# Optimization experiments

Measured on AMD Instinct MI355X. Metric: run time of the kernel, lower is better.

## Reference

```python
import jax, jax.numpy as jnp
import numpy as np

# ---- quantization constants (8-bit, per-tensor affine; representative values) ----
Q_MAX = 255.0
S_IN, Z_IN = 0.05, 128.0      # block input
S1, Z1 = 0.04, 128.0          # after expand 1x1 + hardswish
S2, Z2 = 0.04, 128.0          # after depthwise 5x5 + hardswish
S_SE1, Z_SE1 = 0.03, 128.0    # SE fc1 output
S_SE2, Z_SE2 = 1.0 / 255.0, 0.0  # SE fc2 hardsigmoid output in [0,1]
S_MUL, Z_MUL = 0.04, 128.0    # SE gated activation
S3, Z3 = 0.05, 128.0          # after project 1x1
S_OUT, Z_OUT = 0.06, 128.0    # after residual add
W_SCALE = 0.01                # symmetric per-tensor weight scale (zero_point = 0)
EXP_C = 576                   # expanded channels (depthwise groups)


def conv(x, w, stride=1, padding=0, groups=1):
    return jax.lax.conv_general_dilated(
        x, w, (stride, stride), [(padding, padding), (padding, padding)],
        feature_group_count=groups, dimension_numbers=('NCHW', 'OIHW', 'NCHW'))


def hardswish(x):
    return x * jnp.clip(x + 3.0, 0.0, 6.0) * (1.0 / 6.0)


def hardsigmoid(x):
    return jnp.clip(x + 3.0, 0.0, 6.0) * (1.0 / 6.0)


def qconv(x_q, w_q, b_q, s_in, z_in, s_out, z_out, stride=1, padding=0, groups=1, act=None):
    """Quantized conv: int-domain accumulation (simulated in fp32), fused activation
    on the dequantized accumulator, then requantize to [0, Q_MAX]."""
    acc = conv(x_q - z_in, w_q, stride, padding, groups) + b_q[None, :, None, None]
    deq = acc * (s_in * W_SCALE)  # dequantize accumulator
    if act == 'hardswish':
        deq = hardswish(deq)
    elif act == 'hardsigmoid':
        deq = hardsigmoid(deq)
    return jnp.clip(deq * (1.0 / s_out) + z_out, 0.0, Q_MAX)


def setup_inputs() -> dict:
    key = jax.random.key(0)
    ks = jax.random.split(key, 11)
    def qw(k, shape):  # int8-style symmetric weights stored as fp32 integers
        return jnp.round(jnp.clip(jax.random.normal(k, shape) * 40.0, -127.0, 127.0))
    def qb(k, n):      # int32-style bias in accumulator domain
        return jnp.round(jax.random.normal(k, (n,)) * 500.0)
    return {
        'x':      jnp.round(jax.random.uniform(ks[0], (64, 96, 28, 28)) * Q_MAX),
        'w_exp':  qw(ks[1], (576, 96, 1, 1)),  'b_exp':  qb(ks[2], 576),
        'w_dw':   qw(ks[3], (576, 1, 5, 5)),   'b_dw':   qb(ks[4], 576),
        'w_se1':  qw(ks[5], (144, 576, 1, 1)), 'b_se1':  qb(ks[6], 144),
        'w_se2':  qw(ks[7], (576, 144, 1, 1)), 'b_se2':  qb(ks[8], 576),
        'w_proj': qw(ks[9], (96, 576, 1, 1)),  'b_proj': qb(ks[10], 96),
    }


def reference(x, w_exp, b_exp, w_dw, b_dw, w_se1, b_se1, w_se2, b_se2, w_proj, b_proj):
    # expand 1x1 (+ hardswish)
    e = qconv(x, w_exp, b_exp, S_IN, Z_IN, S1, Z1, act='hardswish')
    # depthwise 5x5, padding=(5-1)//2=2, groups=expanded (+ hardswish)
    d = qconv(e, w_dw, b_dw, S1, Z1, S2, Z2, padding=2, groups=EXP_C, act='hardswish')
    # squeeze-excitation: global avg pool -> fc1 -> fc2(hardsigmoid) -> quantized mul
    pooled = jnp.mean(d, axis=(2, 3), keepdims=True)  # [N, 576, 1, 1]
    g1 = qconv(pooled, w_se1, b_se1, S2, Z2, S_SE1, Z_SE1)
    g2 = qconv(g1, w_se2, b_se2, S_SE1, Z_SE1, S_SE2, Z_SE2, act='hardsigmoid')
    gated = jnp.clip((g2 - Z_SE2) * (d - Z2) * (S_SE2 * S2 / S_MUL) + Z_MUL, 0.0, Q_MAX)
    # project 1x1 (linear)
    p = qconv(gated, w_proj, b_proj, S_MUL, Z_MUL, S3, Z3)
    # quantized residual add (stride=1, in==out channels -> use_res_connect)
    out = jnp.clip((x - Z_IN) * (S_IN / S_OUT) + (p - Z3) * (S3 / S_OUT) + Z_OUT, 0.0, Q_MAX)
    return out
```

## Files before the change

### kernel.cpp

```cpp
#include <hip/hip_runtime.h>

typedef _Float16 v8h __attribute__((ext_vector_type(8)));
typedef _Float16 v4h __attribute__((ext_vector_type(4)));
typedef _Float16 v2h __attribute__((ext_vector_type(2)));
typedef float v4f __attribute__((ext_vector_type(4)));

#define NB 64
#define CI 96
#define CE 576
#define CO 96
#define HW 784
#define SEC 144

#if defined(__has_builtin)
#if __has_builtin(__builtin_amdgcn_fdot2)
#define HAVE_FDOT2 1
#endif
#endif

__device__ __forceinline__ float fdot2(v2h a, v2h b, float c) {
#ifdef HAVE_FDOT2
  return __builtin_amdgcn_fdot2(a, b, c, false);
#else
  return (float)a[0] * (float)b[0] + ((float)a[1] * (float)b[1] + c);
#endif
}

__device__ __forceinline__ float clampf(float x, float lo, float hi) {
#if defined(__has_builtin)
#if __has_builtin(__builtin_amdgcn_fmed3f)
  return __builtin_amdgcn_fmed3f(x, lo, hi);
#else
  return fminf(fmaxf(x, lo), hi);
#endif
#else
  return fminf(fmaxf(x, lo), hi);
#endif
}

__global__ __launch_bounds__(256) void k0_pack_cvt(const float* __restrict__ x,
                                                   _Float16* __restrict__ x_f,
                                                   const float* __restrict__ w_exp,
                                                   const float* __restrict__ w_proj,
                                                   _Float16* __restrict__ w_exp_h,
                                                   _Float16* __restrict__ w_proj_h) {
  __shared__ _Float16 xl[112][104];
  const int tid = threadIdx.x;

  if (blockIdx.y == NB) {
    for (int i = blockIdx.x * 256 + tid; i < CE * CI; i += 7 * 256) {
      w_exp_h[i]  = (_Float16)w_exp[i];
      w_proj_h[i] = (_Float16)w_proj[i];
    }
    return;
  }

  const int n = blockIdx.y;
  const int hw0 = blockIdx.x * 112;

  for (int idx = tid; idx < CI * 28; idx += 256) {
    int c = idx / 28, seg = idx % 28;
    const float4 v = *(const float4*)&x[(n * CI + c) * HW + hw0 + seg * 4];
    int row = seg * 4;
    xl[row + 0][c] = (_Float16)(v.x - 128.0f);
    xl[row + 1][c] = (_Float16)(v.y - 128.0f);
    xl[row + 2][c] = (_Float16)(v.z - 128.0f);
    xl[row + 3][c] = (_Float16)(v.w - 128.0f);
  }
  __syncthreads();

  for (int idx = tid; idx < 1344; idx += 256) {
    int t_l = idx / 192, rem = idx % 192, s = rem / 64, ln = rem % 64;
    int hw_l = t_l * 16 + (ln & 15), ci = s * 32 + (ln >> 4) * 8;
    v8h o;
#pragma unroll
    for (int j = 0; j < 8; ++j) o[j] = xl[hw_l][ci + j];
    size_t t = (size_t)(blockIdx.x * 7 + t_l);
    *(v8h*)&x_f[(((size_t)n * 49 + t) * 3 + s) * 512 + ln * 8] = o;
  }
}

__global__ __launch_bounds__(512, 8) void k12_fused(const _Float16* __restrict__ x_f,
                                                    const _Float16* __restrict__ w_exp_h,
                                                    const float* __restrict__ b_exp,
                                                    const float* __restrict__ w_dw,
                                                    const float* __restrict__ b_dw,
                                                    _Float16* __restrict__ d_t,
                                                    float* __restrict__ d_sums2) {
  __shared__ _Float16 e_lds[16][18][38];
  __shared__ _Float16 d_tile[16][394];
  __shared__ _Float16 w_pairs[16][5][8];
  const int tid = threadIdx.x;

  const int flat = blockIdx.x + 36 * blockIdx.y + 72 * blockIdx.z;
  const int xcd = flat & 7, slot = flat >> 3;
  const int nl = slot / 72, w72 = slot - nl * 72;
  const int n = xcd * 8 + nl;
  const int h = w72 / 36;
  const int c0 = (w72 - h * 36) * 16;

  {
    unsigned long long* z = (unsigned long long*)&e_lds[0][0][0];
    for (int idx = tid; idx < 16 * 18 * 38 * 2 / 8; idx += 512) z[idx] = 0ull;
  }
  for (int idx = tid; idx < 640; idx += 512) {
    int c = idx / 40, r = idx % 40, dy = r / 8, k = r % 8;
    int tap = (k < 4) ? k : (k - 3);
    w_pairs[c][dy][k] = (_Float16)w_dw[(c0 + c) * 25 + dy * 5 + tap];
  }
  __syncthreads();

  const int wv = tid >> 6, lane = tid & 63;
  const int l15 = lane & 15, q = lane >> 4;

  {
    const _Float16* wrow = &w_exp_h[(c0 + l15) * CI + q * 8];
    v8h a0 = *(const v8h*)(wrow);
    v8h a1 = *(const v8h*)(wrow + 32);
    v8h a2 = *(const v8h*)(wrow + 64);
    float bia3[4], bia2[4];
#pragma unroll
    for (int r = 0; r < 4; ++r) {
      float b = b_exp[c0 + q * 4 + r];
      bia3[r] = fmaf(b, 5.0e-4f, 3.0f);
      bia2[r] = b * (5.0e-4f * 25.0f / 6.0f);
    }

    const int ir0 = 14 * h - 2;
    const _Float16* xb = x_f + (size_t)n * (49 * 3 * 512) + lane * 8;
    int hw0 = (21 * h + wv) * 16 + l15;
    int y = hw0 / 28;
    int xx = hw0 - y * 28;
#pragma unroll
    for (int it = 0; it < 4; ++it) {
      int t_l = wv + it * 8;
      if (t_l < 28) {
        int t = 21 * h + t_l;
        const _Float16* xt = xb + (size_t)t * (3 * 512);
        v8h b0 = *(const v8h*)(xt);
        v8h b1 = *(const v8h*)(xt + 512);
        v8h b2 = *(const v8h*)(xt + 1024);
        v4f acc = (v4f){0.f, 0.f, 0.f, 0.f};
        acc = __builtin_amdgcn_mfma_f32_16x16x32_f16(a0, b0, acc, 0, 0, 0);
        acc = __builtin_amdgcn_mfma_f32_16x16x32_f16(a1, b1, acc, 0, 0, 0);
        acc = __builtin_amdgcn_mfma_f32_16x16x32_f16(a2, b2, acc, 0, 0, 0);
        _Float16* dst = &e_lds[q * 4][y - ir0][6 + xx];
#pragma unroll
        for (int r = 0; r < 4; ++r) {
          float t1  = fmaf(acc[r], 5.0e-4f, bia3[r]);
          float cl  = clampf(t1, 0.0f, 6.0f);
          float a2v = fmaf(acc[r], 5.0e-4f * 25.0f / 6.0f, bia2[r]);
          float ev  = clampf(a2v * cl, -128.0f, 127.0f);
          dst[r * (18 * 38)] = (_Float16)ev;
        }
      }
      xx += 16; y += 4;
      if (xx >= 28) { xx -= 28; ++y; }
    }
  }
  __syncthreads();

  const int c = tid >> 5, l = tid & 31;
  v2h W01[5], W23[5], W12[5], W34[5];
  float W0s[5], W4s[5];
#pragma unroll
  for (int dy = 0; dy < 5; ++dy) {
    W01[dy] = *(const v2h*)&w_pairs[c][dy][0];
    W23[dy] = *(const v2h*)&w_pairs[c][dy][2];
    W12[dy] = *(const v2h*)&w_pairs[c][dy][4];
    W34[dy] = *(const v2h*)&w_pairs[c][dy][6];
    W0s[dy] = (float)W01[dy][0];
    W4s[dy] = (float)W34[dy][1];
  }
  const float bc = b_dw[c0 + c];

#define DW_REQUANT(oo, dvv)                                                   \
  {                                                                           \
    float t1_ = fmaf((oo), 4.0e-4f, 3.0f);                                    \
    float cl_ = clampf(t1_, 0.0f, 6.0f);                                      \
    dvv = clampf((oo) * (4.0e-4f * 25.0f / 6.0f) * cl_, -128.0f, 127.0f);     \
  }

  float csum = 0.0f;
  if (l < 28) {
    const int ry = l >> 1;
    const int bx = (l & 1) * 14;
    v2h P0[5], P1[5], P2[5], P3[5];
#pragma unroll
    for (int dy = 0; dy < 5; ++dy) {
      const _Float16* row = &e_lds[c][ry + dy][bx];
      P0[dy] = *(const v2h*)(row + 4);
      P1[dy] = *(const v2h*)(row + 6);
      P2[dy] = *(const v2h*)(row + 8);
      P3[dy] = *(const v2h*)(row + 10);
    }
#pragma unroll
    for (int xi = 0; xi < 3; ++xi) {
      const int x0 = bx + xi * 4;
      float o0 = bc, o1 = bc, o2 = bc, o3 = bc;
#pragma unroll
      for (int dy = 0; dy < 5; ++dy) {
        o0 = fdot2(P0[dy], W01[dy], o0);
        o0 = fdot2(P1[dy], W23[dy], o0);
        o0 += (float)P2[dy][0] * W4s[dy];
        o1 += (float)P0[dy][1] * W0s[dy];
        o1 = fdot2(P1[dy], W12[dy], o1);
        o1 = fdot2(P2[dy], W34[dy], o1);
        o2 = fdot2(P1[dy], W01[dy], o2);
        o2 = fdot2(P2[dy], W23[dy], o2);
        o2 += (float)P3[dy][0] * W4s[dy];
        o3 += (float)P1[dy][1] * W0s[dy];
        o3 = fdot2(P2[dy], W12[dy], o3);
        o3 = fdot2(P3[dy], W34[dy], o3);
      }
      float d0, d1, d2, d3;
      DW_REQUANT(o0, d0); DW_REQUANT(o1, d1);
      DW_REQUANT(o2, d2); DW_REQUANT(o3, d3);
      csum += (d0 + d1) + (d2 + d3);
      v2h dva, dvb;
      dva[0] = (_Float16)d0; dva[1] = (_Float16)d1;
      dvb[0] = (_Float16)d2; dvb[1] = (_Float16)d3;
      *(v2h*)&d_tile[c][ry * 28 + x0]     = dva;
      *(v2h*)&d_tile[c][ry * 28 + x0 + 2] = dvb;
#pragma unroll
      for (int dy = 0; dy < 5; ++dy) {
        const _Float16* row = &e_lds[c][ry + dy][bx];
        P0[dy] = P2[dy];
        P1[dy] = P3[dy];
        P2[dy] = *(const v2h*)(row + x0 - bx + 12);
        P3[dy] = *(const v2h*)(row + x0 - bx + 14);
      }
    }
    {
      float o0 = bc, o1 = bc;
#pragma unroll
      for (int dy = 0; dy < 5; ++dy) {
        o0 = fdot2(P0[dy], W01[dy], o0);
        o0 = fdot2(P1[dy], W23[dy], o0);
        o0 += (float)P2[dy][0] * W4s[dy];
        o1 += (float)P0[dy][1] * W0s[dy];
        o1 = fdot2(P1[dy], W12[dy], o1);
        o1 = fdot2(P2[dy], W34[dy], o1);
      }
      float d0, d1;
      DW_REQUANT(o0, d0); DW_REQUANT(o1, d1);
      csum += d0 + d1;
      v2h dv; dv[0] = (_Float16)d0; dv[1] = (_Float16)d1;
      *(v2h*)&d_tile[c][ry * 28 + bx + 12] = dv;
    }
  }
#pragma unroll
  for (int m = 16; m >= 1; m >>= 1) csum += __shfl_xor(csum, m);
  if (l == 0) d_sums2[((size_t)h * NB + n) * CE + c0 + c] = csum;

  __syncthreads();
  const size_t obase = ((size_t)n * 72 + (c0 >> 3)) * 784 + 392 * h;
  if (tid < 392) {
    int hw_l = tid;
    v8h o0, o1;
#pragma unroll
    for (int j = 0; j < 8; ++j) { o0[j] = d_tile[j][hw_l]; o1[j] = d_tile[8 + j][hw_l]; }
    *(v8h*)&d_t[(obase + hw_l) * 8] = o0;
    *(v8h*)&d_t[(obase + 784 + hw_l) * 8] = o1;
  }
}

__global__ __launch_bounds__(256) void k3a_fc1(const float* __restrict__ d_sums2,
                                               const float* __restrict__ w_se1,
                                               const float* __restrict__ b_se1,
                                               float* __restrict__ g1) {
  const int tid = threadIdx.x;
  const int wv = tid >> 6, lane = tid & 63;
  const int n = blockIdx.y;
  const int o = blockIdx.x * 4 + wv;
  const float* wrow = &w_se1[o * CE];
  const float* s0 = &d_sums2[(size_t)n * CE];
  const float* s1 = &d_sums2[((size_t)NB + n) * CE];
  float p = 0.f;
#pragma unroll
  for (int s = 0; s < 9; ++s) {
    int cc = lane + s * 64;
    p = fmaf(wrow[cc], s0[cc] + s1[cc], p);
  }
#pragma unroll
  for (int m = 32; m >= 1; m >>= 1) p += __shfl_xor(p, m);
  if (lane == 0) {
    g1[n * SEC + o] = clampf(fmaf(p, 1.0f / 58800.0f,
                                  fmaf(b_se1[o], 1.0f / 75.0f, 128.0f)),
                             0.0f, 255.0f) - 128.0f;
  }
}

__global__ __launch_bounds__(256) void k3b_fc2(const float* __restrict__ g1,
                                               const float* __restrict__ w_se2,
                                               const float* __restrict__ b_se2,
                                               _Float16* __restrict__ g2h) {
  const int tid = threadIdx.x;
  const int wv = tid >> 6, lane = tid & 63;
  const int n = blockIdx.y;
  const int o = blockIdx.x * 4 + wv;
  const float* wrow = &w_se2[o * SEC];
  const float* grow = &g1[n * SEC];
  float p = fmaf(wrow[lane], grow[lane], wrow[lane + 64] * grow[lane + 64]);
  if (lane < 16) p = fmaf(wrow[lane + 128], grow[lane + 128], p);
#pragma unroll
  for (int m = 32; m >= 1; m >>= 1) p += __shfl_xor(p, m);
  if (lane == 0) {
    float t = fmaf(p, 3.0e-4f, fmaf(b_se2[o], 3.0e-4f, 3.0f));
    g2h[n * CE + o] = (_Float16)(clampf(t, 0.0f, 6.0f) * (1.0f / 6.0f));
  }
}

__global__ __launch_bounds__(192) void k4_proj(const _Float16* __restrict__ d_t,
                                               const _Float16* __restrict__ g2h,
                                               const _Float16* __restrict__ w_proj_h,
                                               const float* __restrict__ b_proj,
                                               const float* __restrict__ x,
                                               float* __restrict__ out) {
  const int tid = threadIdx.x;

  const int flat = blockIdx.x + 7 * blockIdx.y + 14 * blockIdx.z;
  const int xcd = flat & 7, slot = flat >> 3;
  const int nl = slot / 14, w14 = slot - nl * 14;
  const int n = xcd * 8 + nl;
  const int byy = w14 / 7;
  const int co0 = byy * 48;
  const int hw0 = (w14 - byy * 7) * 112;

  const int wv = tid >> 6, lane = tid & 63;
  const int l15 = lane & 15, q = lane >> 4;

  v4f acc[7];
#pragma unroll
  for (int t = 0; t < 7; ++t) acc[t] = (v4f){0.f, 0.f, 0.f, 0.f};

  const _Float16* dbase = d_t + (((size_t)n * 72 + q) * 784 + hw0 + l15) * 8;
  const _Float16* abase = &w_proj_h[(co0 + wv * 16 + l15) * CE + q * 8];
  const _Float16* gbase = &g2h[(size_t)n * CE + q * 8];

#define K4_LOAD(SUF, KS)                                                      \
  {                                                                           \
    const int ks_ = (KS);                                                     \
    a##SUF = *(const v8h*)(abase + ks_ * 32);                                 \
    g##SUF = *(const v8h*)(gbase + ks_ * 32);                                 \
    const _Float16* dk_ = dbase + (size_t)ks_ * (4 * 784 * 8);                \
    _Pragma("unroll")                                                         \
    for (int t = 0; t < 7; ++t) b##SUF[t] = *(const v8h*)(dk_ + t * (16 * 8));\
  }
#define K4_COMPUTE(SUF)                                                       \
  {                                                                           \
    v8h ag_ = a##SUF * g##SUF;                                                \
    _Pragma("unroll")                                                         \
    for (int t = 0; t < 7; ++t)                                               \
      acc[t] = __builtin_amdgcn_mfma_f32_16x16x32_f16(ag_, b##SUF[t],         \
                                                      acc[t], 0, 0, 0);       \
  }

  v8h aA, gA, bA[7], aB, gB, bB[7];
  K4_LOAD(A, 0);
#pragma unroll
  for (int ks = 0; ks < 18; ks += 2) {
    K4_LOAD(B, ks + 1);
    K4_COMPUTE(A);
    if (ks + 2 < 18) K4_LOAD(A, ks + 2);
    K4_COMPUTE(B);
  }

  float biaf[4];
#pragma unroll
  for (int r = 0; r < 4; ++r)
    biaf[r] = fmaf(b_proj[co0 + wv * 16 + q * 4 + r], 8.0e-3f, 128.0f);

#pragma unroll
  for (int t = 0; t < 7; ++t) {
#pragma unroll
    for (int r = 0; r < 4; ++r) {
      int co = co0 + wv * 16 + q * 4 + r;
      int hw = hw0 + t * 16 + l15;
      float p  = clampf(fmaf(acc[t][r], 8.0e-3f, biaf[r]), 0.0f, 255.0f);
      float xv = x[(n * CO + co) * HW + hw];
      float o = fmaf(xv + p, 0.8333333333f, -85.33333333f);
      out[(n * CO + co) * HW + hw] = clampf(o, 0.0f, 255.0f);
    }
  }
}

extern "C" void kernel_launch(void* const* d_in, const int* in_sizes, int n_in,
                              void* d_out, int out_size, void* d_ws, size_t ws_size,
                              hipStream_t stream) {
  const float* x      = (const float*)d_in[0];
  const float* w_exp  = (const float*)d_in[1];
  const float* b_exp  = (const float*)d_in[2];
  const float* w_dw   = (const float*)d_in[3];
  const float* b_dw   = (const float*)d_in[4];
  const float* w_se1  = (const float*)d_in[5];
  const float* b_se1  = (const float*)d_in[6];
  const float* w_se2  = (const float*)d_in[7];
  const float* b_se2  = (const float*)d_in[8];
  const float* w_proj = (const float*)d_in[9];
  const float* b_proj = (const float*)d_in[10];
  float* out = (float*)d_out;

  char* ws = (char*)d_ws;
  const size_t SZ_W  = (size_t)CE * CI * 2;
  const size_t SZ_XF = (size_t)NB * 49 * 3 * 512 * 2;
  const size_t SZ_D  = (size_t)NB * CE * HW * 2;
  const size_t SZ_S2 = (size_t)2 * NB * CE * 4;
  const size_t SZ_S  = (size_t)NB * CE * 4;
  _Float16* w_exp_h  = (_Float16*)(ws);
  _Float16* w_proj_h = (_Float16*)(ws + SZ_W);
  _Float16* x_f      = (_Float16*)(ws + 2 * SZ_W);
  _Float16* d_t      = (_Float16*)(ws + 2 * SZ_W + SZ_XF);
  float*    d_sums2  = (float*)   (ws + 2 * SZ_W + SZ_XF + SZ_D);
  float*    g1       = (float*)   (ws + 2 * SZ_W + SZ_XF + SZ_D + SZ_S2);
  _Float16* g2h      = (_Float16*)(ws + 2 * SZ_W + SZ_XF + SZ_D + SZ_S2 + SZ_S);

  k0_pack_cvt<<<dim3(7, NB + 1), 256, 0, stream>>>(x, x_f, w_exp, w_proj, w_exp_h, w_proj_h);
  k12_fused<<<dim3(36, 2, NB), 512, 0, stream>>>(x_f, w_exp_h, b_exp, w_dw, b_dw, d_t, d_sums2);
  k3a_fc1<<<dim3(36, NB), 256, 0, stream>>>(d_sums2, w_se1, b_se1, g1);
  k3b_fc2<<<dim3(144, NB), 256, 0, stream>>>(g1, w_se2, b_se2, g2h);
  k4_proj<<<dim3(7, 2, NB), 192, 0, stream>>>(d_t, g2h, w_proj_h, b_proj, x, out);
}
```

Before: 171.2 us.

## Shrink projection tiles to one MFMA tile and drop XCD remap in fused kernel

The projection kernel now gives each block a 16-column spatial tile instead of 112 columns, launching seven times more blocks, each with a single accumulator. The aim is more parallelism and fewer registers per wave. The cost is that weight and gate loads are repeated for every small tile and each thread does less work to hide load latency. The fused expand/depthwise kernel also drops its XCD-aware block remapping in favour of direct block indices, and its d_tile padding shrinks from 394 to 392, which may change LDS bank conflicts.

```diff
diff --git a/kernel.cpp b/kernel.cpp
--- a/kernel.cpp
+++ b/kernel.cpp
@@ -88,16 +88,12 @@
                                                     _Float16* __restrict__ d_t,
                                                     float* __restrict__ d_sums2) {
   __shared__ _Float16 e_lds[16][18][38];
-  __shared__ _Float16 d_tile[16][394];
+  __shared__ _Float16 d_tile[16][392];
   __shared__ _Float16 w_pairs[16][5][8];
   const int tid = threadIdx.x;
-
-  const int flat = blockIdx.x + 36 * blockIdx.y + 72 * blockIdx.z;
-  const int xcd = flat & 7, slot = flat >> 3;
-  const int nl = slot / 72, w72 = slot - nl * 72;
-  const int n = xcd * 8 + nl;
-  const int h = w72 / 36;
-  const int c0 = (w72 - h * 36) * 16;
+  const int n = blockIdx.z;
+  const int h = blockIdx.y;
+  const int c0 = blockIdx.x * 16;
 
   {
     unsigned long long* z = (unsigned long long*)&e_lds[0][0][0];
@@ -319,20 +315,18 @@
                                                float* __restrict__ out) {
   const int tid = threadIdx.x;
 
-  const int flat = blockIdx.x + 7 * blockIdx.y + 14 * blockIdx.z;
+  const int flat = blockIdx.x + 49 * blockIdx.y + 98 * blockIdx.z;
   const int xcd = flat & 7, slot = flat >> 3;
-  const int nl = slot / 14, w14 = slot - nl * 14;
+  const int nl = slot / 98, w98 = slot - nl * 98;
   const int n = xcd * 8 + nl;
-  const int byy = w14 / 7;
+  const int byy = w98 / 49;
   const int co0 = byy * 48;
-  const int hw0 = (w14 - byy * 7) * 112;
+  const int hw0 = (w98 - byy * 49) * 16;
 
   const int wv = tid >> 6, lane = tid & 63;
   const int l15 = lane & 15, q = lane >> 4;
 
-  v4f acc[7];
-#pragma unroll
-  for (int t = 0; t < 7; ++t) acc[t] = (v4f){0.f, 0.f, 0.f, 0.f};
+  v4f acc = (v4f){0.f, 0.f, 0.f, 0.f};
 
   const _Float16* dbase = d_t + (((size_t)n * 72 + q) * 784 + hw0 + l15) * 8;
   const _Float16* abase = &w_proj_h[(co0 + wv * 16 + l15) * CE + q * 8];
@@ -343,20 +337,15 @@
     const int ks_ = (KS);                                                     \
     a##SUF = *(const v8h*)(abase + ks_ * 32);                                 \
     g##SUF = *(const v8h*)(gbase + ks_ * 32);                                 \
-    const _Float16* dk_ = dbase + (size_t)ks_ * (4 * 784 * 8);                \
-    _Pragma("unroll")                                                         \
-    for (int t = 0; t < 7; ++t) b##SUF[t] = *(const v8h*)(dk_ + t * (16 * 8));\
+    b##SUF = *(const v8h*)(dbase + (size_t)ks_ * (4 * 784 * 8));              \
   }
 #define K4_COMPUTE(SUF)                                                       \
   {                                                                           \
     v8h ag_ = a##SUF * g##SUF;                                                \
-    _Pragma("unroll")                                                         \
-    for (int t = 0; t < 7; ++t)                                               \
-      acc[t] = __builtin_amdgcn_mfma_f32_16x16x32_f16(ag_, b##SUF[t],         \
-                                                      acc[t], 0, 0, 0);       \
-  }
-
-  v8h aA, gA, bA[7], aB, gB, bB[7];
+    acc = __builtin_amdgcn_mfma_f32_16x16x32_f16(ag_, b##SUF, acc, 0, 0, 0);  \
+  }
+
+  v8h aA, gA, bA, aB, gB, bB;
   K4_LOAD(A, 0);
 #pragma unroll
   for (int ks = 0; ks < 18; ks += 2) {
@@ -366,22 +355,15 @@
     K4_COMPUTE(B);
   }
 
-  float biaf[4];
-#pragma unroll
-  for (int r = 0; r < 4; ++r)
-    biaf[r] = fmaf(b_proj[co0 + wv * 16 + q * 4 + r], 8.0e-3f, 128.0f);
-
-#pragma unroll
-  for (int t = 0; t < 7; ++t) {
-#pragma unroll
-    for (int r = 0; r < 4; ++r) {
-      int co = co0 + wv * 16 + q * 4 + r;
-      int hw = hw0 + t * 16 + l15;
-      float p  = clampf(fmaf(acc[t][r], 8.0e-3f, biaf[r]), 0.0f, 255.0f);
-      float xv = x[(n * CO + co) * HW + hw];
-      float o = fmaf(xv + p, 0.8333333333f, -85.33333333f);
-      out[(n * CO + co) * HW + hw] = clampf(o, 0.0f, 255.0f);
-    }
+#pragma unroll
+  for (int r = 0; r < 4; ++r) {
+    int co = co0 + wv * 16 + q * 4 + r;
+    int hw = hw0 + l15;
+    float p  = clampf(fmaf(acc[r], 8.0e-3f,
+                           fmaf(b_proj[co], 8.0e-3f, 128.0f)), 0.0f, 255.0f);
+    float xv = x[(n * CO + co) * HW + hw];
+    float o = fmaf(xv + p, 0.8333333333f, -85.33333333f);
+    out[(n * CO + co) * HW + hw] = clampf(o, 0.0f, 255.0f);
   }
 }
 
@@ -419,5 +401,5 @@
   k12_fused<<<dim3(36, 2, NB), 512, 0, stream>>>(x_f, w_exp_h, b_exp, w_dw, b_dw, d_t, d_sums2);
   k3a_fc1<<<dim3(36, NB), 256, 0, stream>>>(d_sums2, w_se1, b_se1, g1);
   k3b_fc2<<<dim3(144, NB), 256, 0, stream>>>(g1, w_se2, b_se2, g2h);
-  k4_proj<<<dim3(7, 2, NB), 192, 0, stream>>>(d_t, g2h, w_proj_h, b_proj, x, out);
-}
+  k4_proj<<<dim3(49, 2, NB), 192, 0, stream>>>(d_t, g2h, w_proj_h, b_proj, x, out);
+}
```

Result: slower. 204.5 us (+19.4%).

## Shrink pack tiles to one 16-pixel tile per block and drop XCD remap

Applied to the files above, without the earlier changes.

The input pack kernel now handles a single 16-pixel tile per block with a grid of 49 tiles per image instead of 7, giving more blocks with a much smaller LDS footprint. The fused expand/depthwise kernel drops its XCD-aware block index remapping in favour of direct blockIdx mapping, and the padding of the d_tile LDS row changes from 394 to 392. This is meant to improve occupancy and parallelism in the pack stage, but it loses the L2 locality the XCD swizzle provided and may add LDS bank conflicts in d_tile.

```diff
diff --git a/kernel.cpp b/kernel.cpp
--- a/kernel.cpp
+++ b/kernel.cpp
@@ -44,11 +44,11 @@
                                                    const float* __restrict__ w_proj,
                                                    _Float16* __restrict__ w_exp_h,
                                                    _Float16* __restrict__ w_proj_h) {
-  __shared__ _Float16 xl[112][104];
+  __shared__ _Float16 xl[16][100];
   const int tid = threadIdx.x;
 
   if (blockIdx.y == NB) {
-    for (int i = blockIdx.x * 256 + tid; i < CE * CI; i += 7 * 256) {
+    for (int i = blockIdx.x * 256 + tid; i < CE * CI; i += 49 * 256) {
       w_exp_h[i]  = (_Float16)w_exp[i];
       w_proj_h[i] = (_Float16)w_proj[i];
     }
@@ -56,26 +56,26 @@
   }
 
   const int n = blockIdx.y;
-  const int hw0 = blockIdx.x * 112;
-
-  for (int idx = tid; idx < CI * 28; idx += 256) {
-    int c = idx / 28, seg = idx % 28;
-    const float4 v = *(const float4*)&x[(n * CI + c) * HW + hw0 + seg * 4];
-    int row = seg * 4;
-    xl[row + 0][c] = (_Float16)(v.x - 128.0f);
-    xl[row + 1][c] = (_Float16)(v.y - 128.0f);
-    xl[row + 2][c] = (_Float16)(v.z - 128.0f);
-    xl[row + 3][c] = (_Float16)(v.w - 128.0f);
+  const int t = blockIdx.x;
+  const int hw0 = t * 16;
+
+  for (int idx = tid; idx < 384; idx += 256) {
+    int ci = idx >> 2, seg = idx & 3;
+    const float4 v = *(const float4*)&x[(n * CI + ci) * HW + hw0 + seg * 4];
+    int r = seg * 4;
+    xl[r + 0][ci] = (_Float16)(v.x - 128.0f);
+    xl[r + 1][ci] = (_Float16)(v.y - 128.0f);
+    xl[r + 2][ci] = (_Float16)(v.z - 128.0f);
+    xl[r + 3][ci] = (_Float16)(v.w - 128.0f);
   }
   __syncthreads();
 
-  for (int idx = tid; idx < 1344; idx += 256) {
-    int t_l = idx / 192, rem = idx % 192, s = rem / 64, ln = rem % 64;
-    int hw_l = t_l * 16 + (ln & 15), ci = s * 32 + (ln >> 4) * 8;
+  if (tid < 192) {
+    int s = tid >> 6, ln = tid & 63;
+    int r = ln & 15, ci = s * 32 + (ln >> 4) * 8;
     v8h o;
 #pragma unroll
-    for (int j = 0; j < 8; ++j) o[j] = xl[hw_l][ci + j];
-    size_t t = (size_t)(blockIdx.x * 7 + t_l);
+    for (int j = 0; j < 8; ++j) o[j] = xl[r][ci + j];
     *(v8h*)&x_f[(((size_t)n * 49 + t) * 3 + s) * 512 + ln * 8] = o;
   }
 }
@@ -88,16 +88,12 @@
                                                     _Float16* __restrict__ d_t,
                                                     float* __restrict__ d_sums2) {
   __shared__ _Float16 e_lds[16][18][38];
-  __shared__ _Float16 d_tile[16][394];
+  __shared__ _Float16 d_tile[16][392];
   __shared__ _Float16 w_pairs[16][5][8];
   const int tid = threadIdx.x;
-
-  const int flat = blockIdx.x + 36 * blockIdx.y + 72 * blockIdx.z;
-  const int xcd = flat & 7, slot = flat >> 3;
-  const int nl = slot / 72, w72 = slot - nl * 72;
-  const int n = xcd * 8 + nl;
-  const int h = w72 / 36;
-  const int c0 = (w72 - h * 36) * 16;
+  const int n = blockIdx.z;
+  const int h = blockIdx.y;
+  const int c0 = blockIdx.x * 16;
 
   {
     unsigned long long* z = (unsigned long long*)&e_lds[0][0][0];
@@ -415,7 +411,7 @@
   float*    g1       = (float*)   (ws + 2 * SZ_W + SZ_XF + SZ_D + SZ_S2);
   _Float16* g2h      = (_Float16*)(ws + 2 * SZ_W + SZ_XF + SZ_D + SZ_S2 + SZ_S);
 
-  k0_pack_cvt<<<dim3(7, NB + 1), 256, 0, stream>>>(x, x_f, w_exp, w_proj, w_exp_h, w_proj_h);
+  k0_pack_cvt<<<dim3(49, NB + 1), 256, 0, stream>>>(x, x_f, w_exp, w_proj, w_exp_h, w_proj_h);
   k12_fused<<<dim3(36, 2, NB), 512, 0, stream>>>(x_f, w_exp_h, b_exp, w_dw, b_dw, d_t, d_sums2);
   k3a_fc1<<<dim3(36, NB), 256, 0, stream>>>(d_sums2, w_se1, b_se1, g1);
   k3b_fc2<<<dim3(144, NB), 256, 0, stream>>>(g1, w_se2, b_se2, g2h);
```

Result: no change. 169.4 us (median of 2 runs) (-1.1%).
